# Kernel tuning notes

Measured on AMD Instinct MI355X. Metric: run time of the kernel, lower is better.

The kernel has to match this reference:

```python
import jax, jax.numpy as jnp
import numpy as np

N_NODES = 100000
N_EDGES = 1000000
N_REL = 200
D_IN = 64
D_OUT = 64


def setup_inputs() -> dict:
    key = jax.random.key(0)
    ks = jax.random.split(key, 12)
    scale = float(np.sqrt(6.0 / (D_IN + D_OUT)))  # xavier_uniform
    inp = {
        "node_feat": jax.random.normal(ks[0], (N_NODES, D_IN), dtype=jnp.float32),
        "rel_emb": jax.random.normal(ks[1], (N_REL, D_IN), dtype=jnp.float32),
        "src": jax.random.randint(ks[2], (N_EDGES,), 0, N_NODES, dtype=jnp.int32),
        "dst": jax.random.randint(ks[3], (N_EDGES,), 0, N_NODES, dtype=jnp.int32),
        "etype": jax.random.randint(ks[4], (N_EDGES,), 0, N_REL, dtype=jnp.int32),
        "direction": jax.random.randint(ks[5], (N_EDGES,), 0, 2, dtype=jnp.int32),
        "W_self": jax.random.uniform(ks[6], (D_OUT, D_IN), jnp.float32, -scale, scale),
        "W_forward": jax.random.uniform(ks[7], (D_OUT, D_IN), jnp.float32, -scale, scale),
        "W_backward": jax.random.uniform(ks[8], (D_OUT, D_IN), jnp.float32, -scale, scale),
        "W_rel": jax.random.uniform(ks[9], (D_OUT, D_IN), jnp.float32, -scale, scale),
        "bias": jnp.zeros((D_OUT,), dtype=jnp.float32),
    }
    return inp


def reference(node_feat, rel_emb, src, dst, etype, direction,
              W_self, W_forward, W_backward, W_rel, bias):
    # Gather: edge messages via 'sub' composition (h_src - r_etype). [E, D_in]
    msg = node_feat[src] - rel_emb[etype]
    # Direction-specific linear transform. Torch code only fills msg_transformed
    # for forward (direction==0) edges; backward edges contribute zeros.
    msg_t = msg @ W_forward.T  # [E, D_out]
    fwd_mask = (direction == 0)[:, None].astype(msg_t.dtype)
    msg_t = msg_t * fwd_mask
    # Scatter-reduce (sum) into destination nodes.
    h_neigh = jax.ops.segment_sum(msg_t, dst, num_segments=N_NODES)
    out = node_feat @ W_self.T + h_neigh + bias
    rel_out = rel_emb @ W_rel.T
    return out, rel_out
```

## Files before the change

kernel.cpp:

```cpp
#include <hip/hip_runtime.h>

#define D 64
#define SCAN_CHUNK 1024

typedef short bf16x8 __attribute__((ext_vector_type(8)));
typedef float f32x4 __attribute__((ext_vector_type(4)));

__device__ __forceinline__ short f2bf(float x) {
  unsigned u = __builtin_bit_cast(unsigned, x);
  u = u + 0x7FFFu + ((u >> 16) & 1u);
  return (short)(u >> 16);
}
__device__ __forceinline__ float bf2f(unsigned short u) {
  unsigned v = ((unsigned)u) << 16;
  return __builtin_bit_cast(float, v);
}

__global__ __launch_bounds__(256) void rel_kernel(
    const float* __restrict__ rel_emb,
    const float* __restrict__ W_f,
    const float* __restrict__ W_rel,
    unsigned short* __restrict__ R2,
    float* __restrict__ rel_out,
    int n_rel,
    int4* __restrict__ cz, int ncz4) {
  {
    int i = blockIdx.x * blockDim.x + threadIdx.x;
    int stride = gridDim.x * blockDim.x;
    int4 z = {0, 0, 0, 0};
    for (; i < ncz4; i += stride) cz[i] = z;
  }
  __shared__ float WtF[D][D];
  __shared__ float WtR[D][D];
  int tid = threadIdx.x;
  for (int idx = tid; idx < D * D; idx += 256) {
    int j = idx >> 6, k = idx & 63;
    WtF[k][j] = W_f[idx];
    WtR[k][j] = W_rel[idx];
  }
  __syncthreads();
  int lane = tid & 63, wave = tid >> 6;
  for (int r = blockIdx.x * 4 + wave; r < n_rel; r += gridDim.x * 4) {
    const float4* a = (const float4*)(rel_emb + (size_t)r * D);
    float accR = 0.f, accO = 0.f;
#pragma unroll
    for (int k4 = 0; k4 < 16; ++k4) {
      float4 av = a[k4];
      int k = k4 * 4;
      accR += av.x * WtF[k][lane] + av.y * WtF[k + 1][lane] +
              av.z * WtF[k + 2][lane] + av.w * WtF[k + 3][lane];
      accO += av.x * WtR[k][lane] + av.y * WtR[k + 1][lane] +
              av.z * WtR[k + 2][lane] + av.w * WtR[k + 3][lane];
    }
    R2[(size_t)r * D + lane] = (unsigned short)f2bf(accR);
    rel_out[(size_t)r * D + lane] = accO;
  }
}

__global__ __launch_bounds__(256) void node_mfma(
    const float* __restrict__ nf,
    const float* __restrict__ W_self,
    const float* __restrict__ W_f,
    const float* __restrict__ bias,
    float* __restrict__ out,
    unsigned short* __restrict__ X2,
    int n_nodes) {
  int tid = threadIdx.x;
  int lane = tid & 63;
  int l15 = lane & 15;
  int kg = lane >> 4;

  bf16x8 bS[4][2], bF[4][2];
#pragma unroll
  for (int q = 0; q < 4; ++q) {
#pragma unroll
    for (int h = 0; h < 2; ++h) {
      const float* ps = W_self + (size_t)(q * 16 + l15) * D + h * 32 + kg * 8;
      const float* pf = W_f + (size_t)(q * 16 + l15) * D + h * 32 + kg * 8;
      float4 s0 = *(const float4*)ps, s1 = *(const float4*)(ps + 4);
      float4 f0 = *(const float4*)pf, f1 = *(const float4*)(pf + 4);
      bf16x8 vs, vf;
      vs[0] = f2bf(s0.x); vs[1] = f2bf(s0.y); vs[2] = f2bf(s0.z); vs[3] = f2bf(s0.w);
      vs[4] = f2bf(s1.x); vs[5] = f2bf(s1.y); vs[6] = f2bf(s1.z); vs[7] = f2bf(s1.w);
      vf[0] = f2bf(f0.x); vf[1] = f2bf(f0.y); vf[2] = f2bf(f0.z); vf[3] = f2bf(f0.w);
      vf[4] = f2bf(f1.x); vf[5] = f2bf(f1.y); vf[6] = f2bf(f1.z); vf[7] = f2bf(f1.w);
      bS[q][h] = vs;
      bF[q][h] = vf;
    }
  }
  float bq[4];
#pragma unroll
  for (int q = 0; q < 4; ++q) bq[q] = bias[q * 16 + l15];

  int wave = (int)((blockIdx.x * blockDim.x + tid) >> 6);
  int n_waves = (int)((gridDim.x * blockDim.x) >> 6);
  int ntiles = (n_nodes + 15) >> 4;

  for (int t = wave; t < ntiles; t += n_waves) {
    int base = t << 4;
    int arow = base + l15;
    if (arow >= n_nodes) arow = n_nodes - 1;
    const float* ap = nf + (size_t)arow * D + kg * 8;
    float4 a00 = *(const float4*)ap;
    float4 a01 = *(const float4*)(ap + 4);
    float4 a10 = *(const float4*)(ap + 32);
    float4 a11 = *(const float4*)(ap + 36);
    bf16x8 af0, af1;
    af0[0] = f2bf(a00.x); af0[1] = f2bf(a00.y); af0[2] = f2bf(a00.z); af0[3] = f2bf(a00.w);
    af0[4] = f2bf(a01.x); af0[5] = f2bf(a01.y); af0[6] = f2bf(a01.z); af0[7] = f2bf(a01.w);
    af1[0] = f2bf(a10.x); af1[1] = f2bf(a10.y); af1[2] = f2bf(a10.z); af1[3] = f2bf(a10.w);
    af1[4] = f2bf(a11.x); af1[5] = f2bf(a11.y); af1[6] = f2bf(a11.z); af1[7] = f2bf(a11.w);

    bool full = (base + 16 <= n_nodes);
#pragma unroll
    for (int q = 0; q < 4; ++q) {
      f32x4 accS = {0.f, 0.f, 0.f, 0.f};
      f32x4 accF = {0.f, 0.f, 0.f, 0.f};
      accS = __builtin_amdgcn_mfma_f32_16x16x32_bf16(af0, bS[q][0], accS, 0, 0, 0);
      accS = __builtin_amdgcn_mfma_f32_16x16x32_bf16(af1, bS[q][1], accS, 0, 0, 0);
      accF = __builtin_amdgcn_mfma_f32_16x16x32_bf16(af0, bF[q][0], accF, 0, 0, 0);
      accF = __builtin_amdgcn_mfma_f32_16x16x32_bf16(af1, bF[q][1], accF, 0, 0, 0);
      int col = q * 16 + l15;
      int row0 = base + kg * 4;
      size_t o = (size_t)row0 * D + col;
      if (full) {
#pragma unroll
        for (int r = 0; r < 4; ++r) {
          out[o + (size_t)r * D] = accS[r] + bq[q];
          X2[o + (size_t)r * D] = (unsigned short)f2bf(accF[r]);
        }
      } else {
#pragma unroll
        for (int r = 0; r < 4; ++r) {
          if (row0 + r < n_nodes) {
            out[o + (size_t)r * D] = accS[r] + bq[q];
            X2[o + (size_t)r * D] = (unsigned short)f2bf(accF[r]);
          }
        }
      }
    }
  }
}

__global__ __launch_bounds__(256) void k_hist(
    const int* __restrict__ dst, const int* __restrict__ dir,
    int* __restrict__ cnt, int n_edges) {
  int i = blockIdx.x * blockDim.x + threadIdx.x;
  int stride = gridDim.x * blockDim.x;
  for (; i < n_edges; i += stride)
    if (dir[i] == 0) atomicAdd(&cnt[dst[i]], 1);
}

__global__ __launch_bounds__(256) void k_sums(
    const int* __restrict__ cnt, int* __restrict__ sums, int n) {
  __shared__ int ws_[4];
  int b = blockIdx.x, t = threadIdx.x;
  int lane = t & 63, wave = t >> 6;
  int s = 0;
  for (int j = 0; j < 4; ++j) {
    int i = b * SCAN_CHUNK + t * 4 + j;
    if (i < n) s += cnt[i];
  }
  for (int off = 32; off; off >>= 1) s += __shfl_down(s, off);
  if (lane == 0) ws_[wave] = s;
  __syncthreads();
  if (t == 0) sums[b] = ws_[0] + ws_[1] + ws_[2] + ws_[3];
}

__global__ __launch_bounds__(256) void k_scan_chunks(
    int* __restrict__ cnt, const int* __restrict__ sums, int n) {
  __shared__ int wsum[4];
  __shared__ int off_s;
  int b = blockIdx.x, t = threadIdx.x;
  int lane = t & 63, wave = t >> 6;
  if (t < 64) {
    int v = 0;
    for (int i = t; i < b; i += 64) v += sums[i];
    for (int o = 32; o; o >>= 1) v += __shfl_down(v, o);
    if (t == 0) off_s = v;
  }
  int i0 = b * SCAN_CHUNK + t * 4;
  int c0 = (i0 + 0 < n) ? cnt[i0 + 0] : 0;
  int c1 = (i0 + 1 < n) ? cnt[i0 + 1] : 0;
  int c2 = (i0 + 2 < n) ? cnt[i0 + 2] : 0;
  int c3 = (i0 + 3 < n) ? cnt[i0 + 3] : 0;
  int s = c0 + c1 + c2 + c3;
  int inc = s;
  for (int d = 1; d < 64; d <<= 1) {
    int v = __shfl_up(inc, d);
    if (lane >= d) inc += v;
  }
  if (lane == 63) wsum[wave] = inc;
  __syncthreads();
  int wbase = 0;
  if (wave > 0) wbase += wsum[0];
  if (wave > 1) wbase += wsum[1];
  if (wave > 2) wbase += wsum[2];
  int ex = off_s + wbase + inc - s;
  if (i0 + 0 < n) cnt[i0 + 0] = ex;
  if (i0 + 1 < n) cnt[i0 + 1] = ex + c0;
  if (i0 + 2 < n) cnt[i0 + 2] = ex + c0 + c1;
  if (i0 + 3 < n) cnt[i0 + 3] = ex + c0 + c1 + c2;
}

__global__ __launch_bounds__(256) void k_scatter_packed(
    const int* __restrict__ src, const int* __restrict__ dst,
    const int* __restrict__ et, const int* __restrict__ dir,
    int* __restrict__ cursor, int* __restrict__ perm, int n_edges) {
  int i = blockIdx.x * blockDim.x + threadIdx.x;
  int stride = gridDim.x * blockDim.x;
  for (; i < n_edges; i += stride)
    if (dir[i] == 0) {
      int pos = atomicAdd(&cursor[dst[i]], 1);
      perm[pos] = (src[i] << 8) | et[i];
    }
}

__global__ __launch_bounds__(256) void k_gather(
    const int* __restrict__ cursor, const int* __restrict__ perm,
    const unsigned short* __restrict__ X2, const unsigned short* __restrict__ R2,
    float* __restrict__ out, int n_nodes) {
  int lane = threadIdx.x & 63;
  int wave_id = (int)((blockIdx.x * blockDim.x + threadIdx.x) >> 6);
  int n_waves = (int)((gridDim.x * blockDim.x) >> 6);
  for (int node = wave_id; node < n_nodes; node += n_waves) {
    int end = cursor[node];
    int beg = (node == 0) ? 0 : cursor[node - 1];
    if (end <= beg) continue;
    float acc = 0.f;
    int k = beg;
    for (; k + 3 < end; k += 4) {
      int p0 = perm[k], p1 = perm[k + 1], p2 = perm[k + 2], p3 = perm[k + 3];
      float a0 = bf2f(X2[(size_t)(p0 >> 8) * D + lane]) - bf2f(R2[(size_t)(p0 & 255) * D + lane]);
      float a1 = bf2f(X2[(size_t)(p1 >> 8) * D + lane]) - bf2f(R2[(size_t)(p1 & 255) * D + lane]);
      float a2 = bf2f(X2[(size_t)(p2 >> 8) * D + lane]) - bf2f(R2[(size_t)(p2 & 255) * D + lane]);
      float a3 = bf2f(X2[(size_t)(p3 >> 8) * D + lane]) - bf2f(R2[(size_t)(p3 & 255) * D + lane]);
      acc += (a0 + a1) + (a2 + a3);
    }
    for (; k < end; ++k) {
      int p = perm[k];
      acc += bf2f(X2[(size_t)(p >> 8) * D + lane]) - bf2f(R2[(size_t)(p & 255) * D + lane]);
    }
    out[(size_t)node * D + lane] += acc;
  }
}

__global__ __launch_bounds__(256) void edge_atomic(
    const int* __restrict__ src, const int* __restrict__ dst,
    const int* __restrict__ et, const int* __restrict__ dir,
    const unsigned short* __restrict__ X2, const unsigned short* __restrict__ R2,
    float* __restrict__ out, int n_edges) {
  int lane = threadIdx.x & 63;
  long long wave_id = ((long long)blockIdx.x * blockDim.x + threadIdx.x) >> 6;
  long long n_waves = ((long long)gridDim.x * blockDim.x) >> 6;
  for (long long base = wave_id * 64; base < n_edges; base += n_waves * 64) {
    int e = (int)base + lane;
    int s_l = 0, d_l = 0, t_l = 0, dir_l = 1;
    if (e < n_edges) {
      s_l = src[e]; d_l = dst[e]; t_l = et[e]; dir_l = dir[e];
    }
    int cnt = min(64, n_edges - (int)base);
    for (int i = 0; i < cnt; ++i) {
      int dir_i = __shfl(dir_l, i);
      if (dir_i != 0) continue;
      int s_i = __shfl(s_l, i);
      int t_i = __shfl(t_l, i);
      int d_i = __shfl(d_l, i);
      float val = bf2f(X2[(size_t)s_i * D + lane]) - bf2f(R2[(size_t)t_i * D + lane]);
      atomicAdd(&out[(size_t)d_i * D + lane], val);
    }
  }
}

extern "C" void kernel_launch(void* const* d_in, const int* in_sizes, int n_in,
                              void* d_out, int out_size, void* d_ws, size_t ws_size,
                              hipStream_t stream) {
  const float* node_feat = (const float*)d_in[0];
  const float* rel_emb   = (const float*)d_in[1];
  const int*   src       = (const int*)d_in[2];
  const int*   dst       = (const int*)d_in[3];
  const int*   etype     = (const int*)d_in[4];
  const int*   direction = (const int*)d_in[5];
  const float* W_self    = (const float*)d_in[6];
  const float* W_forward = (const float*)d_in[7];
  const float* W_rel     = (const float*)d_in[9];
  const float* bias      = (const float*)d_in[10];

  int n_nodes = in_sizes[0] / D;
  int n_rel   = in_sizes[1] / D;
  int n_edges = in_sizes[2];

  float* out     = (float*)d_out;
  float* rel_out = out + (size_t)n_nodes * D;

  char* ws = (char*)d_ws;
  size_t offX = 0;
  size_t offR = offX + (size_t)n_nodes * D * 2;
  size_t offCur = offR + (size_t)n_rel * D * 2;
  offCur = (offCur + 15) & ~(size_t)15;
  size_t offSums = offCur + (((size_t)n_nodes * 4 + 15) & ~(size_t)15);
  size_t offPerm = offSums + 1024 * 4;
  size_t need = offPerm + (size_t)n_edges * 4;

  unsigned short* X2 = (unsigned short*)(ws + offX);
  unsigned short* R2 = (unsigned short*)(ws + offR);
  int* cursor = (int*)(ws + offCur);
  int* sums = (int*)(ws + offSums);
  int* perm = (int*)(ws + offPerm);

  bool packed_ok = (n_rel <= 256) && (n_nodes < (1 << 23));
  bool csr = (ws_size >= need) && packed_ok;
  int ncz4 = csr ? (n_nodes + 3) / 4 : 0;

  rel_kernel<<<64, 256, 0, stream>>>(rel_emb, W_forward, W_rel, R2, rel_out,
                                     n_rel, (int4*)cursor, ncz4);

  node_mfma<<<512, 256, 0, stream>>>(node_feat, W_self, W_forward, bias,
                                     out, X2, n_nodes);

  if (csr) {
    int nblk = (n_nodes + SCAN_CHUNK - 1) / SCAN_CHUNK;
    k_hist<<<1024, 256, 0, stream>>>(dst, direction, cursor, n_edges);
    k_sums<<<nblk, 256, 0, stream>>>(cursor, sums, n_nodes);
    k_scan_chunks<<<nblk, 256, 0, stream>>>(cursor, sums, n_nodes);
    k_scatter_packed<<<1024, 256, 0, stream>>>(src, dst, etype, direction,
                                               cursor, perm, n_edges);
    k_gather<<<2048, 256, 0, stream>>>(cursor, perm, X2, R2, out, n_nodes);
  } else {
    edge_atomic<<<2048, 256, 0, stream>>>(src, dst, etype, direction, X2, R2,
                                          out, n_edges);
  }
}
```

Before: 124.5 us.

## Fuse scan kernels, vectorize histogram and scatter loads, widen gather grid

Replaces the two-pass chunk-sum plus scan with a single scan kernel. In it, each block recomputes its prefix offset by summing all preceding counts with int4 loads, and it writes the cursors to a separate buffer so the counts stay intact. The histogram and scatter kernels now load four edges at a time as int4 vectors. The gather tail is unrolled and its grid is doubled. Dropping one launch and cutting per-edge load instructions trades against redundant prefix reads, which grow quadratically with block index.

```diff
diff --git a/kernel.cpp b/kernel.cpp
--- a/kernel.cpp
+++ b/kernel.cpp
@@ -147,38 +147,44 @@
     int* __restrict__ cnt, int n_edges) {
   int i = blockIdx.x * blockDim.x + threadIdx.x;
   int stride = gridDim.x * blockDim.x;
-  for (; i < n_edges; i += stride)
-    if (dir[i] == 0) atomicAdd(&cnt[dst[i]], 1);
-}
-
-__global__ __launch_bounds__(256) void k_sums(
-    const int* __restrict__ cnt, int* __restrict__ sums, int n) {
-  __shared__ int ws_[4];
-  int b = blockIdx.x, t = threadIdx.x;
-  int lane = t & 63, wave = t >> 6;
-  int s = 0;
-  for (int j = 0; j < 4; ++j) {
-    int i = b * SCAN_CHUNK + t * 4 + j;
-    if (i < n) s += cnt[i];
-  }
-  for (int off = 32; off; off >>= 1) s += __shfl_down(s, off);
-  if (lane == 0) ws_[wave] = s;
-  __syncthreads();
-  if (t == 0) sums[b] = ws_[0] + ws_[1] + ws_[2] + ws_[3];
-}
-
-__global__ __launch_bounds__(256) void k_scan_chunks(
-    int* __restrict__ cnt, const int* __restrict__ sums, int n) {
+  int nv = n_edges >> 2;
+  const int4* d4 = (const int4*)dst;
+  const int4* r4 = (const int4*)dir;
+  for (int v = i; v < nv; v += stride) {
+    int4 d = d4[v];
+    int4 r = r4[v];
+    if (r.x == 0) atomicAdd(&cnt[d.x], 1);
+    if (r.y == 0) atomicAdd(&cnt[d.y], 1);
+    if (r.z == 0) atomicAdd(&cnt[d.z], 1);
+    if (r.w == 0) atomicAdd(&cnt[d.w], 1);
+  }
+  for (int e = (nv << 2) + i; e < n_edges; e += stride)
+    if (dir[e] == 0) atomicAdd(&cnt[dst[e]], 1);
+}
+
+__global__ __launch_bounds__(256) void k_scan_fused(
+    const int* __restrict__ cnt, int* __restrict__ cursor2, int n) {
   __shared__ int wsum[4];
   __shared__ int off_s;
   int b = blockIdx.x, t = threadIdx.x;
   int lane = t & 63, wave = t >> 6;
-  if (t < 64) {
+
+  {
     int v = 0;
-    for (int i = t; i < b; i += 64) v += sums[i];
+    const int4* c4 = (const int4*)cnt;
+    int lim4 = (b * SCAN_CHUNK) >> 2;
+    for (int i = t; i < lim4; i += 256) {
+      int4 c = c4[i];
+      v += c.x + c.y + c.z + c.w;
+    }
     for (int o = 32; o; o >>= 1) v += __shfl_down(v, o);
-    if (t == 0) off_s = v;
-  }
+    if (lane == 0) wsum[wave] = v;
+    __syncthreads();
+    if (t == 0) off_s = wsum[0] + wsum[1] + wsum[2] + wsum[3];
+    __syncthreads();
+  }
+  __syncthreads();
+
   int i0 = b * SCAN_CHUNK + t * 4;
   int c0 = (i0 + 0 < n) ? cnt[i0 + 0] : 0;
   int c1 = (i0 + 1 < n) ? cnt[i0 + 1] : 0;
@@ -197,10 +203,10 @@
   if (wave > 1) wbase += wsum[1];
   if (wave > 2) wbase += wsum[2];
   int ex = off_s + wbase + inc - s;
-  if (i0 + 0 < n) cnt[i0 + 0] = ex;
-  if (i0 + 1 < n) cnt[i0 + 1] = ex + c0;
-  if (i0 + 2 < n) cnt[i0 + 2] = ex + c0 + c1;
-  if (i0 + 3 < n) cnt[i0 + 3] = ex + c0 + c1 + c2;
+  if (i0 + 0 < n) cursor2[i0 + 0] = ex;
+  if (i0 + 1 < n) cursor2[i0 + 1] = ex + c0;
+  if (i0 + 2 < n) cursor2[i0 + 2] = ex + c0 + c1;
+  if (i0 + 3 < n) cursor2[i0 + 3] = ex + c0 + c1 + c2;
 }
 
 __global__ __launch_bounds__(256) void k_scatter_packed(
@@ -209,10 +215,25 @@
     int* __restrict__ cursor, int* __restrict__ perm, int n_edges) {
   int i = blockIdx.x * blockDim.x + threadIdx.x;
   int stride = gridDim.x * blockDim.x;
-  for (; i < n_edges; i += stride)
-    if (dir[i] == 0) {
-      int pos = atomicAdd(&cursor[dst[i]], 1);
-      perm[pos] = (src[i] << 8) | et[i];
+  int nv = n_edges >> 2;
+  const int4* s4 = (const int4*)src;
+  const int4* d4 = (const int4*)dst;
+  const int4* t4 = (const int4*)et;
+  const int4* r4 = (const int4*)dir;
+  for (int v = i; v < nv; v += stride) {
+    int4 s = s4[v];
+    int4 d = d4[v];
+    int4 tt = t4[v];
+    int4 r = r4[v];
+    if (r.x == 0) perm[atomicAdd(&cursor[d.x], 1)] = (s.x << 8) | tt.x;
+    if (r.y == 0) perm[atomicAdd(&cursor[d.y], 1)] = (s.y << 8) | tt.y;
+    if (r.z == 0) perm[atomicAdd(&cursor[d.z], 1)] = (s.z << 8) | tt.z;
+    if (r.w == 0) perm[atomicAdd(&cursor[d.w], 1)] = (s.w << 8) | tt.w;
+  }
+  for (int e = (nv << 2) + i; e < n_edges; e += stride)
+    if (dir[e] == 0) {
+      int pos = atomicAdd(&cursor[dst[e]], 1);
+      perm[pos] = (src[e] << 8) | et[e];
     }
 }
 
@@ -237,7 +258,13 @@
       float a3 = bf2f(X2[(size_t)(p3 >> 8) * D + lane]) - bf2f(R2[(size_t)(p3 & 255) * D + lane]);
       acc += (a0 + a1) + (a2 + a3);
     }
-    for (; k < end; ++k) {
+    if (k + 1 < end) {
+      int p0 = perm[k], p1 = perm[k + 1];
+      acc += bf2f(X2[(size_t)(p0 >> 8) * D + lane]) - bf2f(R2[(size_t)(p0 & 255) * D + lane]);
+      acc += bf2f(X2[(size_t)(p1 >> 8) * D + lane]) - bf2f(R2[(size_t)(p1 & 255) * D + lane]);
+      k += 2;
+    }
+    if (k < end) {
       int p = perm[k];
       acc += bf2f(X2[(size_t)(p >> 8) * D + lane]) - bf2f(R2[(size_t)(p & 255) * D + lane]);
     }
@@ -296,16 +323,15 @@
   char* ws = (char*)d_ws;
   size_t offX = 0;
   size_t offR = offX + (size_t)n_nodes * D * 2;
-  size_t offCur = offR + (size_t)n_rel * D * 2;
-  offCur = (offCur + 15) & ~(size_t)15;
-  size_t offSums = offCur + (((size_t)n_nodes * 4 + 15) & ~(size_t)15);
-  size_t offPerm = offSums + 1024 * 4;
+  size_t offCnt = (offR + (size_t)n_rel * D * 2 + 15) & ~(size_t)15;
+  size_t offCur2 = offCnt + (((size_t)n_nodes * 4 + 15) & ~(size_t)15);
+  size_t offPerm = offCur2 + (((size_t)n_nodes * 4 + 15) & ~(size_t)15);
   size_t need = offPerm + (size_t)n_edges * 4;
 
   unsigned short* X2 = (unsigned short*)(ws + offX);
   unsigned short* R2 = (unsigned short*)(ws + offR);
-  int* cursor = (int*)(ws + offCur);
-  int* sums = (int*)(ws + offSums);
+  int* cnt = (int*)(ws + offCnt);
+  int* cursor2 = (int*)(ws + offCur2);
   int* perm = (int*)(ws + offPerm);
 
   bool packed_ok = (n_rel <= 256) && (n_nodes < (1 << 23));
@@ -313,19 +339,18 @@
   int ncz4 = csr ? (n_nodes + 3) / 4 : 0;
 
   rel_kernel<<<64, 256, 0, stream>>>(rel_emb, W_forward, W_rel, R2, rel_out,
-                                     n_rel, (int4*)cursor, ncz4);
+                                     n_rel, (int4*)cnt, ncz4);
 
   node_mfma<<<512, 256, 0, stream>>>(node_feat, W_self, W_forward, bias,
                                      out, X2, n_nodes);
 
   if (csr) {
     int nblk = (n_nodes + SCAN_CHUNK - 1) / SCAN_CHUNK;
-    k_hist<<<1024, 256, 0, stream>>>(dst, direction, cursor, n_edges);
-    k_sums<<<nblk, 256, 0, stream>>>(cursor, sums, n_nodes);
-    k_scan_chunks<<<nblk, 256, 0, stream>>>(cursor, sums, n_nodes);
+    k_hist<<<1024, 256, 0, stream>>>(dst, direction, cnt, n_edges);
+    k_scan_fused<<<nblk, 256, 0, stream>>>(cnt, cursor2, n_nodes);
     k_scatter_packed<<<1024, 256, 0, stream>>>(src, dst, etype, direction,
-                                               cursor, perm, n_edges);
-    k_gather<<<2048, 256, 0, stream>>>(cursor, perm, X2, R2, out, n_nodes);
+                                               cursor2, perm, n_edges);
+    k_gather<<<4096, 256, 0, stream>>>(cursor2, perm, X2, R2, out, n_nodes);
   } else {
     edge_atomic<<<2048, 256, 0, stream>>>(src, dst, etype, direction, X2, R2,
                                           out, n_edges);
```

Measured after the change: 132.6 us. 1.07x slower.
